# Performance work log

Measured on AMD Instinct MI355X. Metric: run time of the kernel, lower is better.

The kernel has to match this reference:

```python
import jax, jax.numpy as jnp
import numpy as np

B, T, D, H = 2, 2048, 1024, 16
HD = D // H  # head_dim = 64


def apply_rope(x, cos, sin):
    # x: [B, H, T, HD]; cos/sin: [1, 1, T, HD//2]
    x1, x2 = x[..., ::2], x[..., 1::2]
    y1 = x1 * cos - x2 * sin
    y2 = x1 * sin + x2 * cos
    # interleave back: [..., HD//2, 2] -> [..., HD]
    return jnp.stack([y1, y2], axis=-1).reshape(x.shape)


def setup_inputs() -> dict:
    key = jax.random.key(0)
    ks = jax.random.split(key, 11)
    s = 0.02
    return {
        "x": jax.random.normal(ks[0], (B, T, D), jnp.float32),
        "cos": jax.random.normal(ks[1], (1, 1, T, HD // 2), jnp.float32),
        "sin": jax.random.normal(ks[2], (1, 1, T, HD // 2), jnp.float32),
        "Wq": jax.random.normal(ks[3], (D, D), jnp.float32) * s,
        "bq": jax.random.normal(ks[4], (D,), jnp.float32) * s,
        "Wk": jax.random.normal(ks[5], (D, D), jnp.float32) * s,
        "bk": jax.random.normal(ks[6], (D,), jnp.float32) * s,
        "Wv": jax.random.normal(ks[7], (D, D), jnp.float32) * s,
        "bv": jax.random.normal(ks[8], (D,), jnp.float32) * s,
        "Wo": jax.random.normal(ks[9], (D, D), jnp.float32) * s,
        "bo": jax.random.normal(ks[10], (D,), jnp.float32) * s,
    }


def reference(x, cos, sin, Wq, bq, Wk, bk, Wv, bv, Wo, bo):
    b, t, d = x.shape
    # projections (nn.Linear: x @ W.T + b)
    q = (x @ Wq.T + bq).reshape(b, t, H, HD).transpose(0, 2, 1, 3)
    k = (x @ Wk.T + bk).reshape(b, t, H, HD).transpose(0, 2, 1, 3)
    v = (x @ Wv.T + bv).reshape(b, t, H, HD).transpose(0, 2, 1, 3)
    q = apply_rope(q, cos, sin)
    k = apply_rope(k, cos, sin)
    scores = jnp.einsum("bhqd,bhkd->bhqk", q, k) / jnp.sqrt(jnp.asarray(HD, x.dtype))
    # causal mask: query i attends to keys j <= i
    causal = jnp.tril(jnp.ones((t, t), dtype=bool))
    scores = jnp.where(causal, scores, jnp.asarray(-jnp.inf, x.dtype))
    weights = jax.nn.softmax(scores, axis=-1)
    out = jnp.einsum("bhqk,bhkd->bhqd", weights, v)
    out = out.transpose(0, 2, 1, 3).reshape(b, t, d)
    return out @ Wo.T + bo
```

## Files before the change

kernel.cpp:

```cpp
#include <hip/hip_runtime.h>
#include <hip/hip_bf16.h>
#include <cstdint>
#include <cstddef>

typedef __attribute__((ext_vector_type(8))) short bf16x8;
typedef __attribute__((ext_vector_type(4))) float f32x4;
typedef __attribute__((ext_vector_type(16))) float f32x16;

#define SCALE2 0.180336880111112f
#define VSTRIDE 2080

__device__ __forceinline__ unsigned short f2bf(float f) {
    unsigned u = __builtin_bit_cast(unsigned, f);
    unsigned r = (u + 0x7FFFu + ((u >> 16) & 1u)) >> 16;
    return (unsigned short)r;
}

__device__ __forceinline__ void gload16(const unsigned short* g, unsigned short* l) {
    __builtin_amdgcn_global_load_lds(
        (const __attribute__((address_space(1))) unsigned int*)(g),
        (__attribute__((address_space(3))) unsigned int*)(l), 16, 0, 0);
}

__global__ void cvt_all(const float* __restrict__ x,
                        const float* __restrict__ wq, const float* __restrict__ wk,
                        const float* __restrict__ wv, const float* __restrict__ wo,
                        unsigned short* __restrict__ xb,
                        unsigned short* __restrict__ wqb, unsigned short* __restrict__ wkb,
                        unsigned short* __restrict__ wvb, unsigned short* __restrict__ wob)
{
    const int y = blockIdx.y;
    const float* src; unsigned short* dst; int n;
    switch (y) {
        case 0: src = x;  dst = xb;  n = 4194304; break;
        case 1: src = wq; dst = wqb; n = 1048576; break;
        case 2: src = wk; dst = wkb; n = 1048576; break;
        case 3: src = wv; dst = wvb; n = 1048576; break;
        default: src = wo; dst = wob; n = 1048576; break;
    }
    const int i = (blockIdx.x * 256 + threadIdx.x) * 4;
    if (i < n) {
        float4 v = *(const float4*)(src + i);
        ushort4 o;
        o.x = f2bf(v.x); o.y = f2bf(v.y); o.z = f2bf(v.z); o.w = f2bf(v.w);
        *(ushort4*)(dst + i) = o;
    }
}

__global__ __launch_bounds__(256) void gemm_qkv(
    const unsigned short* __restrict__ xb,
    const unsigned short* __restrict__ wqb,
    const unsigned short* __restrict__ wkb,
    const unsigned short* __restrict__ wvb,
    const float* __restrict__ bq, const float* __restrict__ bk, const float* __restrict__ bv,
    const float* __restrict__ cosT, const float* __restrict__ sinT,
    unsigned short* __restrict__ Qb, unsigned short* __restrict__ Kb, unsigned short* __restrict__ Vtg)
{
    const int bid = blockIdx.x;
    const int xcd = bid & 7;
    const int s = bid >> 3;
    const int i4 = xcd >> 1, k2 = xcd & 1;
    const int z = s >> 5;
    const int tt = s & 31;
    const int m0 = (i4 * 8 + (tt >> 2)) * 128;
    const int n0 = (k2 * 4 + (tt & 3)) * 128;

    const unsigned short* wb = (z == 0) ? wqb : ((z == 1) ? wkb : wvb);
    const float* bias = (z == 0) ? bq : ((z == 1) ? bk : bv);
    unsigned short* dst = (z == 0) ? Qb : Kb;

    __shared__ __align__(16) unsigned short Al[128 * 32];
    __shared__ __align__(16) unsigned short Bl[128 * 32];
    __shared__ __align__(16) unsigned short Ct[128 * 136];

    const int tid = threadIdx.x;
    const int lane = tid & 63;
    const int w = tid >> 6;
    const int wr = w >> 1, wc = w & 1;
    const int lr = lane & 15, lg = lane >> 4;
    const int srow = tid >> 2, sseg = tid & 3;
    const int wbase = tid & 192;

    f32x4 acc[4][4] = {};

    for (int k0 = 0; k0 < 1024; k0 += 32) {
        __syncthreads();
#pragma unroll
        for (int p = 0; p < 2; ++p) {
            const int row = srow + p * 64;
            gload16(xb + (size_t)(m0 + row) * 1024 + k0 + sseg * 8, Al + (p * 256 + wbase) * 8);
            gload16(wb + (size_t)(n0 + row) * 1024 + k0 + sseg * 8, Bl + (p * 256 + wbase) * 8);
        }
        __syncthreads();
        bf16x8 af[4], bfr[4];
#pragma unroll
        for (int mt = 0; mt < 4; ++mt)
            af[mt] = *(const bf16x8*)(Al + (wr * 64 + mt * 16 + lr) * 32 + lg * 8);
#pragma unroll
        for (int nt = 0; nt < 4; ++nt)
            bfr[nt] = *(const bf16x8*)(Bl + (wc * 64 + nt * 16 + lr) * 32 + lg * 8);
#pragma unroll
        for (int mt = 0; mt < 4; ++mt)
#pragma unroll
            for (int nt = 0; nt < 4; ++nt)
                acc[mt][nt] = __builtin_amdgcn_mfma_f32_16x16x32_bf16(af[mt], bfr[nt], acc[mt][nt], 0, 0, 0);
    }

#pragma unroll
    for (int mt = 0; mt < 4; ++mt) {
#pragma unroll
        for (int nt = 0; nt < 4; ++nt) {
            const int coln = wc * 64 + nt * 16 + lr;
            const int col = n0 + coln;
            const float bcol = bias[col];
            const int hd = col & 63;
#pragma unroll
            for (int r = 0; r < 4; ++r) {
                const int rowm = wr * 64 + mt * 16 + lg * 4 + r;
                float v = acc[mt][nt][r] + bcol;
                if (z < 2) {
                    float part = __shfl_xor(v, 1);
                    const int ttm = (m0 + rowm) & 2047;
                    const int i = hd >> 1;
                    const float cc = cosT[ttm * 32 + i], ss = sinT[ttm * 32 + i];
                    v = (hd & 1) ? (part * ss + v * cc) : (v * cc - part * ss);
                    if (z == 0) v *= SCALE2;
                    Ct[rowm * 136 + coln] = f2bf(v);
                } else {
                    Ct[coln * 136 + rowm] = f2bf(v);
                }
            }
        }
    }
    __syncthreads();
    if (z < 2) {
#pragma unroll
        for (int p = 0; p < 8; ++p) {
            const int u = p * 256 + tid;
            const int row = u >> 4, seg = u & 15;
            bf16x8 vv = *(const bf16x8*)(Ct + row * 136 + seg * 8);
            const int mrow = m0 + row;
            const int ttm = mrow & 2047, bb = mrow >> 11;
            const int col = n0 + seg * 8;
            const int h = col >> 6, hd = col & 63;
            *(bf16x8*)(dst + ((size_t)(bb * 16 + h) * 2048 + ttm) * 64 + hd) = vv;
        }
    } else {
        const int bb = m0 >> 11;
#pragma unroll
        for (int p = 0; p < 8; ++p) {
            const int u = p * 256 + tid;
            const int vrow = u >> 4, seg = u & 15;
            bf16x8 vv = *(const bf16x8*)(Ct + vrow * 136 + seg * 8);
            const int col = n0 + vrow;
            const int h = col >> 6, hd = col & 63;
            const int ttm = (m0 + seg * 8) & 2047;
            *(bf16x8*)(Vtg + ((size_t)(bb * 16 + h) * 64 + hd) * VSTRIDE + ttm) = vv;
        }
    }
}

__global__ __launch_bounds__(256, 2) void attn_fwd(
    const unsigned short* __restrict__ Qb, const unsigned short* __restrict__ Kb,
    const unsigned short* __restrict__ Vtg, unsigned short* __restrict__ attnb)
{
    __shared__ __align__(16) unsigned char smem[25088];

    const int tid = threadIdx.x, lane = tid & 63, w = tid >> 6;
    const int l31 = lane & 31, lh = lane >> 5;
    const int bid = blockIdx.x;
    const int bh = bid & 31;
    const int pi = bid >> 5;
    const int half = w >> 1;
    const int slice = w & 1;
    const int cH = 63 - pi;
    const int c = half ? pi : cH;
    const size_t base = (size_t)bh * 131072;
    const int myq = c * 32 + l31;

    const unsigned short* Kg = Kb + base;
    const unsigned short* Vg = Vtg + (size_t)bh * (64 * VSTRIDE);

    bf16x8 qf[4];
#pragma unroll
    for (int s = 0; s < 4; ++s)
        qf[s] = *(const bf16x8*)(Qb + base + (size_t)myq * 64 + s * 16 + lh * 8);

    f32x16 o0 = {}, o1 = {};
    float sm = 0.f;

    const int krow = tid >> 3, kseg = (tid & 7) ^ (krow & 7);
    const int vrow = tid >> 2, vseg = (tid & 3) ^ ((vrow >> 1) & 3);
    const int ldst = (tid & ~63) * 8;

#define STAGE(T, B)                                                                   \
    {                                                                                 \
        unsigned short* kb_ = (unsigned short*)(smem + (B) * 8192);                   \
        unsigned short* vb_ = (unsigned short*)(smem + (B) * 8192 + 4096);            \
        gload16(Kg + (size_t)((T) * 32 + krow) * 64 + kseg * 8, kb_ + ldst);          \
        gload16(Vg + (size_t)vrow * VSTRIDE + (T) * 32 + vseg * 8, vb_ + ldst);       \
    }

    STAGE(0, 0);
    STAGE(1, 1);
    int bsel = 0;
    for (int t = 0; t <= cH; ++t) {
        if (t < cH) asm volatile("s_waitcnt vmcnt(2)" ::: "memory");
        else        asm volatile("s_waitcnt vmcnt(0)" ::: "memory");
        __syncthreads();
        {
            const int t2 = t + 2;
            if (t2 <= cH) {
                int b2 = bsel + 2; if (b2 >= 3) b2 -= 3;
                STAGE(t2, b2);
            }
        }
        if (t <= c && (t & 1) == slice) {
            const unsigned short* Kc = (const unsigned short*)(smem + bsel * 8192);
            const unsigned short* Vc = Kc + 2048;
            const int kvb = t * 32;

            bf16x8 kf0 = *(const bf16x8*)(Kc + l31 * 64 + ((0 * 2 + lh) ^ (l31 & 7)) * 8);
            bf16x8 kf1 = *(const bf16x8*)(Kc + l31 * 64 + ((1 * 2 + lh) ^ (l31 & 7)) * 8);
            bf16x8 kf2 = *(const bf16x8*)(Kc + l31 * 64 + ((2 * 2 + lh) ^ (l31 & 7)) * 8);
            bf16x8 kf3 = *(const bf16x8*)(Kc + l31 * 64 + ((3 * 2 + lh) ^ (l31 & 7)) * 8);

            f32x16 st = {};
            st = __builtin_amdgcn_mfma_f32_32x32x16_bf16(kf0, qf[0], st, 0, 0, 0);
            st = __builtin_amdgcn_mfma_f32_32x32x16_bf16(kf1, qf[1], st, 0, 0, 0);
            st = __builtin_amdgcn_mfma_f32_32x32x16_bf16(kf2, qf[2], st, 0, 0, 0);
            st = __builtin_amdgcn_mfma_f32_32x32x16_bf16(kf3, qf[3], st, 0, 0, 0);

            if (t == c) {
#pragma unroll
                for (int r = 0; r < 16; ++r) {
                    const int kv = kvb + (r & 3) + 8 * (r >> 2) + 4 * lh;
                    st[r] = (kv <= myq) ? st[r] : -1e30f;
                }
            }
#pragma unroll
            for (int r = 0; r < 16; ++r) st[r] = exp2f(st[r]);
            {
                float a0 = st[0] + st[1], a1 = st[2] + st[3];
                float a2 = st[4] + st[5], a3 = st[6] + st[7];
                float a4 = st[8] + st[9], a5 = st[10] + st[11];
                float a6 = st[12] + st[13], a7 = st[14] + st[15];
                sm += ((a0 + a1) + (a2 + a3)) + ((a4 + a5) + (a6 + a7));
            }

            unsigned pw0, pw1, pw2, pw3, pw4, pw5, pw6, pw7;
            {
                unsigned a0, a1, b0, b1;
                asm("v_cvt_pk_bf16_f32 %0, %1, %2" : "=v"(a0) : "v"(st[0]), "v"(st[1]));
                asm("v_cvt_pk_bf16_f32 %0, %1, %2" : "=v"(a1) : "v"(st[2]), "v"(st[3]));
                asm("v_cvt_pk_bf16_f32 %0, %1, %2" : "=v"(b0) : "v"(st[4]), "v"(st[5]));
                asm("v_cvt_pk_bf16_f32 %0, %1, %2" : "=v"(b1) : "v"(st[6]), "v"(st[7]));
                asm("v_permlane32_swap_b32 %0, %1" : "+v"(a0), "+v"(b0));
                asm("v_permlane32_swap_b32 %0, %1" : "+v"(a1), "+v"(b1));
                pw0 = a0; pw1 = a1; pw2 = b0; pw3 = b1;
            }
            {
                unsigned a0, a1, b0, b1;
                asm("v_cvt_pk_bf16_f32 %0, %1, %2" : "=v"(a0) : "v"(st[8]), "v"(st[9]));
                asm("v_cvt_pk_bf16_f32 %0, %1, %2" : "=v"(a1) : "v"(st[10]), "v"(st[11]));
                asm("v_cvt_pk_bf16_f32 %0, %1, %2" : "=v"(b0) : "v"(st[12]), "v"(st[13]));
                asm("v_cvt_pk_bf16_f32 %0, %1, %2" : "=v"(b1) : "v"(st[14]), "v"(st[15]));
                asm("v_permlane32_swap_b32 %0, %1" : "+v"(a0), "+v"(b0));
                asm("v_permlane32_swap_b32 %0, %1" : "+v"(a1), "+v"(b1));
                pw4 = a0; pw5 = a1; pw6 = b0; pw7 = b1;
            }

            const int g0 = (l31 >> 1) & 3;
            bf16x8 vf00 = *(const bf16x8*)(Vc + l31 * 32 + ((lh ^ g0)) * 8);
            bf16x8 vf01 = *(const bf16x8*)(Vc + l31 * 32 + (((2 + lh) ^ g0)) * 8);
            bf16x8 vf10 = *(const bf16x8*)(Vc + (32 + l31) * 32 + ((lh ^ g0)) * 8);
            bf16x8 vf11 = *(const bf16x8*)(Vc + (32 + l31) * 32 + (((2 + lh) ^ g0)) * 8);

            uint4 h0 = make_uint4(pw0, pw1, pw2, pw3);
            uint4 h1 = make_uint4(pw4, pw5, pw6, pw7);
            bf16x8 pf0 = __builtin_bit_cast(bf16x8, h0);
            bf16x8 pf1 = __builtin_bit_cast(bf16x8, h1);
            o0 = __builtin_amdgcn_mfma_f32_32x32x16_bf16(vf00, pf0, o0, 0, 0, 0);
            o1 = __builtin_amdgcn_mfma_f32_32x32x16_bf16(vf10, pf0, o1, 0, 0, 0);
            o0 = __builtin_amdgcn_mfma_f32_32x32x16_bf16(vf01, pf1, o0, 0, 0, 0);
            o1 = __builtin_amdgcn_mfma_f32_32x32x16_bf16(vf11, pf1, o1, 0, 0, 0);
        }
        bsel += 1; if (bsel == 3) bsel = 0;
    }

    sm += __shfl_xor(sm, 32);

    float* Om = (float*)smem;
    float* Ms = (float*)(smem + 16384);
    __syncthreads();
    if (slice == 1) {
#pragma unroll
        for (int i = 0; i < 16; ++i) Om[(half * 32 + i) * 64 + lane] = o0[i];
#pragma unroll
        for (int i = 0; i < 16; ++i) Om[(half * 32 + 16 + i) * 64 + lane] = o1[i];
        Ms[half * 64 + lane] = sm;
    }
    __syncthreads();
    if (slice == 0) {
        const float s = sm + Ms[half * 64 + lane];
        const float inv = 1.f / s;
        const int b = bh >> 4, h = bh & 15;
        unsigned short* obase = attnb + ((size_t)(b * 2048 + myq)) * 1024 + h * 64;
#pragma unroll
        for (int g = 0; g < 4; ++g) {
            ushort4 u;
            u.x = f2bf((o0[g * 4 + 0] + Om[(half * 32 + g * 4 + 0) * 64 + lane]) * inv);
            u.y = f2bf((o0[g * 4 + 1] + Om[(half * 32 + g * 4 + 1) * 64 + lane]) * inv);
            u.z = f2bf((o0[g * 4 + 2] + Om[(half * 32 + g * 4 + 2) * 64 + lane]) * inv);
            u.w = f2bf((o0[g * 4 + 3] + Om[(half * 32 + g * 4 + 3) * 64 + lane]) * inv);
            *(ushort4*)(obase + g * 8 + lh * 4) = u;
            ushort4 v;
            v.x = f2bf((o1[g * 4 + 0] + Om[(half * 32 + 16 + g * 4 + 0) * 64 + lane]) * inv);
            v.y = f2bf((o1[g * 4 + 1] + Om[(half * 32 + 16 + g * 4 + 1) * 64 + lane]) * inv);
            v.z = f2bf((o1[g * 4 + 2] + Om[(half * 32 + 16 + g * 4 + 2) * 64 + lane]) * inv);
            v.w = f2bf((o1[g * 4 + 3] + Om[(half * 32 + 16 + g * 4 + 3) * 64 + lane]) * inv);
            *(ushort4*)(obase + 32 + g * 8 + lh * 4) = v;
        }
    }
#undef STAGE
}

__global__ __launch_bounds__(256) void gemm_out(
    const unsigned short* __restrict__ ab,
    const unsigned short* __restrict__ wob,
    const float* __restrict__ bo,
    float* __restrict__ out)
{
    __shared__ __align__(16) unsigned short Al[128 * 32];
    __shared__ __align__(16) unsigned short Bl[64 * 32];

    const int bid = blockIdx.x;
    const int xcd = bid & 7;
    const int s = bid >> 3;
    const int i4 = xcd >> 1, k2 = xcd & 1;
    const int m0 = (i4 * 8 + (s >> 3)) * 128;
    const int n0 = (k2 * 8 + (s & 7)) * 64;

    const int tid = threadIdx.x;
    const int lane = tid & 63;
    const int w = tid >> 6;
    const int lr = lane & 15, lg = lane >> 4;

    f32x4 acc[2][4] = {};

    for (int k0 = 0; k0 < 1024; k0 += 32) {
        __syncthreads();
#pragma unroll
        for (int p = 0; p < 2; ++p) {
            const int u = p * 256 + tid;
            const int row = u >> 2, seg = u & 3;
            gload16(ab + (size_t)(m0 + row) * 1024 + k0 + seg * 8, Al + (u & ~63) * 8);
        }
        {
            const int u = tid;
            const int row = u >> 2, seg = u & 3;
            gload16(wob + (size_t)(n0 + row) * 1024 + k0 + seg * 8, Bl + (u & ~63) * 8);
        }
        __syncthreads();
        bf16x8 af[2], bfr[4];
#pragma unroll
        for (int mt = 0; mt < 2; ++mt)
            af[mt] = *(const bf16x8*)(Al + (w * 32 + mt * 16 + lr) * 32 + lg * 8);
#pragma unroll
        for (int nt = 0; nt < 4; ++nt)
            bfr[nt] = *(const bf16x8*)(Bl + (nt * 16 + lr) * 32 + lg * 8);
#pragma unroll
        for (int mt = 0; mt < 2; ++mt)
#pragma unroll
            for (int nt = 0; nt < 4; ++nt)
                acc[mt][nt] = __builtin_amdgcn_mfma_f32_16x16x32_bf16(af[mt], bfr[nt], acc[mt][nt], 0, 0, 0);
    }

#pragma unroll
    for (int mt = 0; mt < 2; ++mt) {
#pragma unroll
        for (int nt = 0; nt < 4; ++nt) {
            const int col = n0 + nt * 16 + lr;
            const float bcol = bo[col];
#pragma unroll
            for (int r = 0; r < 4; ++r) {
                const int mrow = m0 + w * 32 + mt * 16 + lg * 4 + r;
                out[(size_t)mrow * 1024 + col] = acc[mt][nt][r] + bcol;
            }
        }
    }
}

extern "C" void kernel_launch(void* const* d_in, const int* in_sizes, int n_in,
                              void* d_out, int out_size, void* d_ws, size_t ws_size,
                              hipStream_t stream) {
    const float* x    = (const float*)d_in[0];
    const float* cosT = (const float*)d_in[1];
    const float* sinT = (const float*)d_in[2];
    const float* Wq   = (const float*)d_in[3];
    const float* bq   = (const float*)d_in[4];
    const float* Wk   = (const float*)d_in[5];
    const float* bk   = (const float*)d_in[6];
    const float* Wv   = (const float*)d_in[7];
    const float* bv   = (const float*)d_in[8];
    const float* Wo   = (const float*)d_in[9];
    const float* bo   = (const float*)d_in[10];
    float* out = (float*)d_out;

    char* ws = (char*)d_ws;
    unsigned short* xb    = (unsigned short*)(ws + 0);
    unsigned short* attnb = (unsigned short*)(ws + 0);
    unsigned short* wob   = (unsigned short*)(ws + 8388608);
    unsigned short* wqb   = (unsigned short*)(ws + 10485760);
    unsigned short* wkb   = (unsigned short*)(ws + 12582912);
    unsigned short* wvb   = (unsigned short*)(ws + 14680064);
    unsigned short* Qb    = (unsigned short*)(ws + 16777216);
    unsigned short* Kb    = (unsigned short*)(ws + 25165824);
    unsigned short* Vtg   = (unsigned short*)(ws + 33554432);

    cvt_all<<<dim3(4096, 5), 256, 0, stream>>>(x, Wq, Wk, Wv, Wo, xb, wqb, wkb, wvb, wob);
    gemm_qkv<<<dim3(768), 256, 0, stream>>>(xb, wqb, wkb, wvb, bq, bk, bv,
                                            cosT, sinT, Qb, Kb, Vtg);
    attn_fwd<<<dim3(1024), 256, 0, stream>>>(Qb, Kb, Vtg, attnb);
    gemm_out<<<dim3(512), 256, 0, stream>>>(attnb, wob, bo, out);
}
```

Before: 118.5 us.

## Stage 64-key K/V tiles per barrier so both slice waves compute each step

The attention loop now loads 64-key tiles of K and V per pipeline stage instead of 32, with each wave slice taking one 32-key half of the tile. The old loop had each wave compute only on alternating iterations. The new loop halves the number of barriers and waitcnt stalls, and both slice wave pairs do useful work in every iteration. In exchange, LDS use roughly doubles to 48 KB for the triple buffer, which may limit occupancy (two blocks per CU are requested). Swizzle patterns are adjusted for the 64-wide rows.

```diff
diff --git a/kernel.cpp b/kernel.cpp
--- a/kernel.cpp
+++ b/kernel.cpp
@@ -164,7 +164,7 @@
     const unsigned short* __restrict__ Qb, const unsigned short* __restrict__ Kb,
     const unsigned short* __restrict__ Vtg, unsigned short* __restrict__ attnb)
 {
-    __shared__ __align__(16) unsigned char smem[25088];
+    __shared__ __align__(16) unsigned char smem[49152];
 
     const int tid = threadIdx.x, lane = tid & 63, w = tid >> 6;
     const int l31 = lane & 31, lh = lane >> 5;
@@ -175,6 +175,7 @@
     const int slice = w & 1;
     const int cH = 63 - pi;
     const int c = half ? pi : cH;
+    const int smax = cH >> 1;
     const size_t base = (size_t)bh * 131072;
     const int myq = c * 32 + l31;
 
@@ -189,41 +190,47 @@
     f32x16 o0 = {}, o1 = {};
     float sm = 0.f;
 
-    const int krow = tid >> 3, kseg = (tid & 7) ^ (krow & 7);
-    const int vrow = tid >> 2, vseg = (tid & 3) ^ ((vrow >> 1) & 3);
-    const int ldst = (tid & ~63) * 8;
-
-#define STAGE(T, B)                                                                   \
+#define STAGE(S, B)                                                                   \
     {                                                                                 \
-        unsigned short* kb_ = (unsigned short*)(smem + (B) * 8192);                   \
-        unsigned short* vb_ = (unsigned short*)(smem + (B) * 8192 + 4096);            \
-        gload16(Kg + (size_t)((T) * 32 + krow) * 64 + kseg * 8, kb_ + ldst);          \
-        gload16(Vg + (size_t)vrow * VSTRIDE + (T) * 32 + vseg * 8, vb_ + ldst);       \
+        unsigned short* kb_ = (unsigned short*)(smem + (B) * 16384);                  \
+        unsigned short* vb_ = (unsigned short*)(smem + (B) * 16384 + 8192);           \
+        _Pragma("unroll")                                                             \
+        for (int p = 0; p < 2; ++p) {                                                 \
+            const int u = p * 256 + tid;                                              \
+            const int row = u >> 3, ss = (u & 7) ^ (row & 7);                         \
+            gload16(Kg + (size_t)((S) * 64 + row) * 64 + ss * 8, kb_ + (u & ~63) * 8);\
+        }                                                                             \
+        _Pragma("unroll")                                                             \
+        for (int p = 0; p < 2; ++p) {                                                 \
+            const int u = p * 256 + tid;                                              \
+            const int row = u >> 3, ss = (u & 7) ^ (row & 7);                         \
+            gload16(Vg + (size_t)row * VSTRIDE + (S) * 64 + ss * 8, vb_ + (u & ~63) * 8);\
+        }                                                                             \
     }
 
     STAGE(0, 0);
     STAGE(1, 1);
     int bsel = 0;
-    for (int t = 0; t <= cH; ++t) {
-        if (t < cH) asm volatile("s_waitcnt vmcnt(2)" ::: "memory");
-        else        asm volatile("s_waitcnt vmcnt(0)" ::: "memory");
+    for (int s = 0; s <= smax; ++s) {
+        if (s < smax) asm volatile("s_waitcnt vmcnt(4)" ::: "memory");
+        else          asm volatile("s_waitcnt vmcnt(0)" ::: "memory");
         __syncthreads();
-        {
-            const int t2 = t + 2;
-            if (t2 <= cH) {
-                int b2 = bsel + 2; if (b2 >= 3) b2 -= 3;
-                STAGE(t2, b2);
-            }
-        }
-        if (t <= c && (t & 1) == slice) {
-            const unsigned short* Kc = (const unsigned short*)(smem + bsel * 8192);
-            const unsigned short* Vc = Kc + 2048;
+        if (s + 2 <= smax) {
+            int b2 = bsel + 2; if (b2 >= 3) b2 -= 3;
+            STAGE(s + 2, b2);
+        }
+        const int t = 2 * s + slice;
+        if (t <= c) {
+            const unsigned short* Kc = (const unsigned short*)(smem + bsel * 16384);
+            const unsigned short* Vc = Kc + 4096;
             const int kvb = t * 32;
-
-            bf16x8 kf0 = *(const bf16x8*)(Kc + l31 * 64 + ((0 * 2 + lh) ^ (l31 & 7)) * 8);
-            bf16x8 kf1 = *(const bf16x8*)(Kc + l31 * 64 + ((1 * 2 + lh) ^ (l31 & 7)) * 8);
-            bf16x8 kf2 = *(const bf16x8*)(Kc + l31 * 64 + ((2 * 2 + lh) ^ (l31 & 7)) * 8);
-            bf16x8 kf3 = *(const bf16x8*)(Kc + l31 * 64 + ((3 * 2 + lh) ^ (l31 & 7)) * 8);
+            const int sw = l31 & 7;
+            const int roff = slice * 32 + l31;
+
+            bf16x8 kf0 = *(const bf16x8*)(Kc + roff * 64 + ((0 + lh) ^ sw) * 8);
+            bf16x8 kf1 = *(const bf16x8*)(Kc + roff * 64 + ((2 + lh) ^ sw) * 8);
+            bf16x8 kf2 = *(const bf16x8*)(Kc + roff * 64 + ((4 + lh) ^ sw) * 8);
+            bf16x8 kf3 = *(const bf16x8*)(Kc + roff * 64 + ((6 + lh) ^ sw) * 8);
 
             f32x16 st = {};
             st = __builtin_amdgcn_mfma_f32_32x32x16_bf16(kf0, qf[0], st, 0, 0, 0);
@@ -270,11 +277,12 @@
                 pw4 = a0; pw5 = a1; pw6 = b0; pw7 = b1;
             }
 
-            const int g0 = (l31 >> 1) & 3;
-            bf16x8 vf00 = *(const bf16x8*)(Vc + l31 * 32 + ((lh ^ g0)) * 8);
-            bf16x8 vf01 = *(const bf16x8*)(Vc + l31 * 32 + (((2 + lh) ^ g0)) * 8);
-            bf16x8 vf10 = *(const bf16x8*)(Vc + (32 + l31) * 32 + ((lh ^ g0)) * 8);
-            bf16x8 vf11 = *(const bf16x8*)(Vc + (32 + l31) * 32 + (((2 + lh) ^ g0)) * 8);
+            const int vs0 = (slice * 4 + lh) ^ sw;
+            const int vs1 = (slice * 4 + 2 + lh) ^ sw;
+            bf16x8 vf00 = *(const bf16x8*)(Vc + l31 * 64 + vs0 * 8);
+            bf16x8 vf01 = *(const bf16x8*)(Vc + l31 * 64 + vs1 * 8);
+            bf16x8 vf10 = *(const bf16x8*)(Vc + (32 + l31) * 64 + vs0 * 8);
+            bf16x8 vf11 = *(const bf16x8*)(Vc + (32 + l31) * 64 + vs1 * 8);
 
             uint4 h0 = make_uint4(pw0, pw1, pw2, pw3);
             uint4 h1 = make_uint4(pw4, pw5, pw6, pw7);
```

Result: no change. 117.3 us (-1.0%).
